# Kernel optimization log

Measured on AMD Instinct MI355X. Metric: run time of the kernel, lower is better.

Reference implementation:

```python
import jax, jax.numpy as jnp
import numpy as np
from jax import lax

B, C, H, W = 32, 256, 56, 56

def _conv(x, w, stride, groups=1, pad='VALID'):
    return lax.conv_general_dilated(x, w, (stride, stride), pad,
                                    feature_group_count=groups,
                                    dimension_numbers=('NCHW', 'OIHW', 'NCHW'))

def _ln(x, g, b, eps=1e-5):
    mu = jnp.mean(x, -1, keepdims=True)
    var = jnp.mean((x - mu) ** 2, -1, keepdims=True)
    return (x - mu) * lax.rsqrt(var + eps) * g + b

def setup_inputs() -> dict:
    key = jax.random.key(0)
    ks = jax.random.split(key, 16)
    s = 0.02
    Ch = C // 2
    d = {}
    d['x'] = jax.random.normal(ks[0], (B, C, H, W), jnp.float32)
    d['Wq'] = jax.random.normal(ks[1], (C, C), jnp.float32) * s;  d['bq'] = jnp.zeros((C,), jnp.float32)
    d['Wk'] = jax.random.normal(ks[2], (C, C), jnp.float32) * s;  d['bk'] = jnp.zeros((C,), jnp.float32)
    d['Wv'] = jax.random.normal(ks[3], (C, C), jnp.float32) * s;  d['bv'] = jnp.zeros((C,), jnp.float32)
    d['sr1_w'] = jax.random.normal(ks[4], (C, C, 8, 8), jnp.float32) * s; d['sr1_b'] = jnp.zeros((C,), jnp.float32)
    d['ln1_g'] = jnp.ones((C,), jnp.float32); d['ln1_b'] = jnp.zeros((C,), jnp.float32)
    d['sr2_w'] = jax.random.normal(ks[5], (C, C, 4, 4), jnp.float32) * s; d['sr2_b'] = jnp.zeros((C,), jnp.float32)
    d['ln2_g'] = jnp.ones((C,), jnp.float32); d['ln2_b'] = jnp.zeros((C,), jnp.float32)
    d['Wkv1'] = jax.random.normal(ks[6], (C, C), jnp.float32) * s; d['bkv1'] = jnp.zeros((C,), jnp.float32)
    d['Wkv2'] = jax.random.normal(ks[7], (C, C), jnp.float32) * s; d['bkv2'] = jnp.zeros((C,), jnp.float32)
    d['lc1_w'] = jax.random.normal(ks[8], (Ch, 1, 3, 3), jnp.float32) * s; d['lc1_b'] = jnp.zeros((Ch,), jnp.float32)
    d['lc2_w'] = jax.random.normal(ks[9], (Ch, 1, 3, 3), jnp.float32) * s; d['lc2_b'] = jnp.zeros((Ch,), jnp.float32)
    d['rp_w'] = jax.random.normal(ks[10], (C, C), jnp.float32) * s;  d['rp_b'] = jnp.zeros((C,), jnp.float32)
    d['rp12_w'] = jax.random.normal(ks[11], (C, C), jnp.float32) * s; d['rp12_b'] = jnp.zeros((C,), jnp.float32)
    d['dw_w'] = jax.random.normal(ks[12], (C, 2), jnp.float32) * 0.5  # Conv3d (2,1,1) depthwise, no bias
    return d

def reference(x, Wq, bq, Wk, bk, Wv, bv, sr1_w, sr1_b, ln1_g, ln1_b,
              sr2_w, sr2_b, ln2_g, ln2_b, Wkv1, bkv1, Wkv2, bkv2,
              lc1_w, lc1_b, lc2_w, lc2_b, rp_w, rp_b, rp12_w, rp12_b, dw_w):
    Bx, Cc, h, w = x.shape
    N = h * w
    Ch = Cc // 2
    xt = x.reshape(Bx, Cc, N).transpose(0, 2, 1)                 # [B,N,C]
    q = jax.nn.softmax(xt @ Wq + bq, axis=-1)                    # softmax over channels
    q1, q2 = q[..., :Ch], q[..., Ch:]

    # spatial-reduction branches (conv -> LN -> GELU)
    x1 = _conv(x, sr1_w, 8) + sr1_b[:, None, None]               # [B,C,7,7]
    x1 = jax.nn.gelu(_ln(x1.reshape(Bx, Cc, -1).transpose(0, 2, 1), ln1_g, ln1_b), approximate=False)
    x2 = _conv(x, sr2_w, 4) + sr2_b[:, None, None]               # [B,C,14,14]
    x2 = jax.nn.gelu(_ln(x2.reshape(Bx, Cc, -1).transpose(0, 2, 1), ln2_g, ln2_b), approximate=False)

    def branch(xr, Wkv, bkv, lc_w, lc_b, qh, hh):
        kv = (xr @ Wkv + bkv).reshape(Bx, -1, 2, Ch)
        k = jax.nn.softmax(kv[:, :, 0], axis=1)                  # softmax over reduced tokens
        v = kv[:, :, 1]
        vsp = v.transpose(0, 2, 1).reshape(Bx, Ch, hh, hh)
        v = v + (_conv(vsp, lc_w, 1, groups=Ch, pad='SAME') + lc_b[:, None, None]).reshape(Bx, Ch, -1).transpose(0, 2, 1)
        ctx = jnp.einsum('bnk,bnv->bkv', k, v)                   # [B,Ch,Ch]
        return jnp.einsum('bnk,bkv->bnv', qh, ctx)               # [B,N,Ch]

    a1 = branch(x1, Wkv1, bkv1, lc1_w, lc1_b, q1, 7)
    a2 = branch(x2, Wkv2, bkv2, lc2_w, lc2_b, q2, 14)
    eff2 = jnp.concatenate([a1, a2], axis=-1)                    # [B,N,C]
    eff2 = jnp.einsum('bni,oi->bon', eff2, rp12_w).reshape(Bx, Cc, h, w) + rp12_b[None, :, None, None]

    # global efficient-attention branch
    keys = jax.nn.softmax(xt @ Wk + bk, axis=1)                  # softmax over tokens
    values = xt @ Wv + bv
    ctx = jnp.einsum('bnk,bnv->bkv', keys, values)               # [B,C,C]
    att = jnp.einsum('bnk,bkv->bnv', q, ctx)                     # [B,N,C]
    eff = jnp.einsum('bni,oi->bon', att, rp_w).reshape(Bx, Cc, h, w) + rp_b[None, :, None, None]

    # Conv3d (2,1,1) depthwise merge over the two branches
    out = eff * dw_w[:, 0][None, :, None, None] + eff2 * dw_w[:, 1][None, :, None, None]
    return out
```

## Files before the change

kernel.cpp:

```cpp
#include <hip/hip_runtime.h>
#include <hip/hip_bf16.h>
#include <math.h>

#define B_ 32
#define H_ 56
#define W_ 56
#define N_ 3136
#define NT_ 100352

typedef short short8 __attribute__((ext_vector_type(8)));
typedef float f32x4 __attribute__((ext_vector_type(4)));

__device__ __forceinline__ unsigned short f2b(float f){
  union { float f; unsigned u; } v; v.f = f;
  return (unsigned short)((v.u + 0x7FFFu + ((v.u>>16)&1u)) >> 16);
}

#define LDSW(row, bo) ((unsigned)((row)*128 + ((bo) ^ (((row)&7)<<4))))

__device__ __forceinline__ short8 ldfrag(const char* base, int row, int kk){
  return *(const short8*)(base + LDSW(row, kk*2));
}
__device__ __forceinline__ f32x4 mfma16(short8 a, short8 b, f32x4 c){
  return __builtin_amdgcn_mfma_f32_16x16x32_bf16(a, b, c, 0, 0, 0);
}
__device__ __forceinline__ void gld16(void* lds, const void* g){
  __builtin_amdgcn_global_load_lds((__attribute__((address_space(1))) void*)g,
                                   (__attribute__((address_space(3))) void*)lds,
                                   16, 0, 0);
}

__global__ void prep_kernel(const float* __restrict__ Wq, const float* __restrict__ Wk,
                            const float* __restrict__ Wv, const float* __restrict__ Wkv1,
                            const float* __restrict__ Wkv2, const float* __restrict__ sr1w,
                            const float* __restrict__ sr2w, const float* __restrict__ rpw,
                            const float* __restrict__ rpb, const float* __restrict__ rp12w,
                            const float* __restrict__ rp12b, const float* __restrict__ dww,
                            unsigned short* WqT, unsigned short* WkT, unsigned short* WvT,
                            unsigned short* Wkv1T, unsigned short* Wkv2T,
                            unsigned short* srw1, unsigned short* srw2,
                            unsigned short* Acomb, float* bias_out)
{
  int idx = blockIdx.x*256 + threadIdx.x;
  const int total = 5*65536 + 4194304 + 1048576 + 131072 + 256;
  for (int i = idx; i < total; i += gridDim.x*256) {
    int j = i;
    if (j < 5*65536) {
      int w = j >> 16, e = j & 65535;
      int o = e >> 8, c = e & 255;
      const float* src = (w==0)?Wq:(w==1)?Wk:(w==2)?Wv:(w==3)?Wkv1:Wkv2;
      unsigned short* dst = (w==0)?WqT:(w==1)?WkT:(w==2)?WvT:(w==3)?Wkv1T:Wkv2T;
      dst[o*256+c] = f2b(src[c*256+o]);
      continue;
    }
    j -= 5*65536;
    if (j < 4194304) {
      int o = j >> 14, rem = j & 16383, pos = rem >> 8, c = rem & 255;
      srw1[j] = f2b(sr1w[o*16384 + c*64 + pos]);
      continue;
    }
    j -= 4194304;
    if (j < 1048576) {
      int o = j >> 12, rem = j & 4095, pos = rem >> 8, c = rem & 255;
      srw2[j] = f2b(sr2w[o*4096 + c*16 + pos]);
      continue;
    }
    j -= 1048576;
    if (j < 131072) {
      int o = j >> 9, i2 = j & 511;
      float v = (i2 < 256) ? dww[o*2+0]*rpw[o*256+i2]
                           : dww[o*2+1]*rp12w[o*256+(i2-256)];
      Acomb[o*512+i2] = f2b(v);
      continue;
    }
    j -= 131072;
    bias_out[j] = dww[j*2+0]*rpb[j] + dww[j*2+1]*rp12b[j];
  }
}

__global__ void transpose_kernel(const float* __restrict__ x, unsigned short* __restrict__ xt)
{
  __shared__ float tile[64][65];
  int bn = blockIdx.x; int b = bn / 49; int n0 = (bn - b*49)*64;
  int c0 = blockIdx.y*64;
  int t = threadIdx.x;
  {
    int cl = t >> 2, nq = t & 3;
    const float* src = x + ((size_t)(b*256 + c0 + cl))*N_ + n0 + nq*16;
#pragma unroll
    for (int j = 0; j < 4; j++){
      float4 v = *(const float4*)(src + j*4);
      tile[cl][nq*16 + j*4 + 0] = v.x;
      tile[cl][nq*16 + j*4 + 1] = v.y;
      tile[cl][nq*16 + j*4 + 2] = v.z;
      tile[cl][nq*16 + j*4 + 3] = v.w;
    }
  }
  __syncthreads();
  {
    int nl = t >> 2, cq = t & 3;
    unsigned short pk[16];
#pragma unroll
    for (int j=0;j<16;j++) pk[j] = f2b(tile[cq*16+j][nl]);
    unsigned short* dst = xt + ((size_t)(b*N_ + n0 + nl))*256 + c0 + cq*16;
    *(uint4*)dst = *(uint4*)&pk[0];
    *(uint4*)(dst+8) = *(uint4*)&pk[8];
  }
}

__global__ __launch_bounds__(256,2) void qkv3_kernel(
    const unsigned short* __restrict__ xt,
    const unsigned short* __restrict__ WqT, const unsigned short* __restrict__ WkT,
    const unsigned short* __restrict__ WvT,
    const float* __restrict__ bq, const float* __restrict__ bk, const float* __restrict__ bv,
    unsigned short* __restrict__ qbuf, unsigned short* __restrict__ KexpT,
    unsigned short* __restrict__ VT, float* __restrict__ s_q, float* __restrict__ s_k)
{
  __shared__ __align__(16) char smem[32768 + 32768 + 1024];
  char* At = smem;
  char* Bt = smem + 32768;
  float* redbuf = (float*)(smem + 65536);
  const int t = threadIdx.x, wave = t>>6, lane = t&63, l15 = lane&15, l4 = lane>>4;
  const int r0 = blockIdx.x*64;
  const int b = r0 / N_;
  const int nl0 = r0 - b*N_;

#pragma unroll
  for (int c4=0;c4<4;c4++)
#pragma unroll
    for (int j=0;j<2;j++){
      int chunk = j*256 + t; int row = chunk>>3, c8 = chunk&7;
      int c8s = c8 ^ (row&7);
      gld16(At + c4*8192 + (j*256 + wave*64)*16,
            xt + (size_t)(r0+row)*256 + c4*64 + c8s*8);
    }
  __syncthreads();

  for (int mat=0; mat<3; mat++){
    const unsigned short* BT = (mat==0)?WqT:(mat==1)?WkT:WvT;
    const float* bias = (mat==0)?bq:(mat==1)?bk:bv;
    const f32x4 vzero = {0.f,0.f,0.f,0.f};
    f32x4 acc[4][4];
#pragma unroll
    for (int i=0;i<4;i++)
#pragma unroll
      for (int j=0;j<4;j++) acc[i][j] = vzero;

    for (int k0c=0;k0c<4;k0c++){
#pragma unroll
      for (int j=0;j<8;j++){
        int chunk = j*256 + t; int row = chunk>>3, c8 = chunk&7;
        int c8s = c8 ^ (row&7);
        gld16(Bt + (j*256 + wave*64)*16, BT + (size_t)row*256 + k0c*64 + c8s*8);
      }
      __syncthreads();
#pragma unroll
      for (int ks=0;ks<2;ks++){
        short8 af[4], bfr[4];
#pragma unroll
        for (int mi=0;mi<4;mi++) af[mi]  = ldfrag(At + k0c*8192, mi*16 + l15, ks*32 + l4*8);
#pragma unroll
        for (int ni=0;ni<4;ni++) bfr[ni] = ldfrag(Bt, wave*64 + ni*16 + l15, ks*32 + l4*8);
#pragma unroll
        for (int mi=0;mi<4;mi++)
#pragma unroll
          for (int ni=0;ni<4;ni++)
            acc[mi][ni] = mfma16(af[mi], bfr[ni], acc[mi][ni]);
      }
      __syncthreads();
    }

    float bb4[4];
#pragma unroll
    for (int ni=0;ni<4;ni++) bb4[ni] = bias[wave*64 + ni*16 + l15];

    if (mat == 0) {
      float rs[4][4];
#pragma unroll
      for (int mi=0;mi<4;mi++)
#pragma unroll
        for (int r=0;r<4;r++) rs[mi][r] = 0.f;
#pragma unroll
      for (int mi=0;mi<4;mi++)
#pragma unroll
        for (int ni=0;ni<4;ni++)
#pragma unroll
          for (int r=0;r<4;r++){
            float e = __expf(acc[mi][ni][r] + bb4[ni]);
            acc[mi][ni][r] = e;
            rs[mi][r] += e;
          }
#pragma unroll
      for (int mi=0;mi<4;mi++)
#pragma unroll
        for (int r=0;r<4;r++){
          float s = rs[mi][r];
          s += __shfl_xor(s, 1); s += __shfl_xor(s, 2);
          s += __shfl_xor(s, 4); s += __shfl_xor(s, 8);
          rs[mi][r] = s;
        }
      if (l15 == 0){
#pragma unroll
        for (int mi=0;mi<4;mi++)
#pragma unroll
          for (int r=0;r<4;r++)
            redbuf[wave*64 + mi*16 + l4*4 + r] = rs[mi][r];
      }
      __syncthreads();
      unsigned short* qb = (unsigned short*)Bt;
#pragma unroll
      for (int mi=0;mi<4;mi++)
#pragma unroll
        for (int r=0;r<4;r++){
          int rr = mi*16 + l4*4 + r;
#pragma unroll
          for (int ni=0;ni<4;ni++)
            qb[rr*256 + wave*64 + ni*16 + l15] = f2b(acc[mi][ni][r]);
        }
      if (t < 64){
        s_q[r0 + t] = redbuf[t] + redbuf[64+t] + redbuf[128+t] + redbuf[192+t];
      }
      __syncthreads();
#pragma unroll
      for (int j=0;j<8;j++){
        int chunk = j*256 + t;
        int row = chunk >> 5, c8 = chunk & 31;
        *(uint4*)(qbuf + (size_t)(r0+row)*256 + c8*8) = *(const uint4*)(qb + row*256 + c8*8);
      }
      __syncthreads();
    } else {
      float cs[4] = {0.f,0.f,0.f,0.f};
#pragma unroll
      for (int mi=0;mi<4;mi++)
#pragma unroll
        for (int ni=0;ni<4;ni++)
#pragma unroll
          for (int r=0;r<4;r++){
            float v = acc[mi][ni][r] + bb4[ni];
            if (mat == 1){ v = __expf(v); cs[ni] += v; }
            int row = mi*16 + l4*4 + r;
            int col = wave*64 + ni*16 + l15;
            *(unsigned short*)(Bt + LDSW(col, row*2)) = f2b(v);
          }
      if (mat == 1){
#pragma unroll
        for (int ni=0;ni<4;ni++){
          float s = cs[ni];
          s += __shfl_xor(s, 16);
          s += __shfl_xor(s, 32);
          if (lane < 16) atomicAdd(&s_k[b*256 + wave*64 + ni*16 + lane], s);
        }
      }
      __syncthreads();
      unsigned short* ot = (mat==1) ? KexpT : VT;
#pragma unroll
      for (int j=0;j<8;j++){
        int chunk = j*256 + t;
        int c = chunk >> 3, n8 = chunk & 7;
        *(uint4*)(ot + ((size_t)b*256 + c)*N_ + nl0 + n8*8) = *(const uint4*)(Bt + LDSW(c, n8*16));
      }
      __syncthreads();
    }
  }
}

template<int S, int OW, int KW, int NSK, int MPB, int KTOT>
__device__ __forceinline__ void srconv_body(
    const unsigned short* __restrict__ xt, const unsigned short* __restrict__ wbf,
    float* __restrict__ part, int bid, char* At, char* Bt)
{
  const int KCH = KTOT / NSK;
  const int Mtot = B_*MPB;
  const int sk = bid % NSK, tile = bid / NSK;
  const int t = threadIdx.x, wave = t>>6, lane = t&63, l15 = lane&15, l4 = lane>>4;
  const f32x4 vzero = {0.f,0.f,0.f,0.f};
  f32x4 acc[4][4];
#pragma unroll
  for (int i=0;i<4;i++)
#pragma unroll
    for (int j=0;j<4;j++) acc[i][j] = vzero;

  size_t abase[2];
#pragma unroll
  for (int j=0;j<2;j++){
    int chunk = j*256 + t;
    int row = chunk >> 3, c8 = chunk & 7;
    int c8s = c8 ^ (row&7);
    int rowc = tile*64 + row; if (rowc > Mtot-1) rowc = Mtot-1;
    int b = rowc / MPB; int m = rowc - b*MPB;
    int p = m / OW; int q = m - p*OW;
    abase[j] = ((size_t)b*N_ + (size_t)(S*p)*W_ + S*q)*256 + c8s*8;
  }

  for (int kt = 0; kt < KCH; kt += 64){
    const int k0 = sk*KCH + kt;
    const int pos = k0 >> 8, cc = k0 & 255;
    const int dy = pos / KW, dx = pos - dy*KW;
    const size_t off = (size_t)(dy*W_ + dx)*256 + cc;
#pragma unroll
    for (int j=0;j<2;j++){
      gld16(At + (j*256 + wave*64)*16, xt + abase[j] + off);
    }
#pragma unroll
    for (int j=0;j<8;j++){
      int chunk = j*256 + t; int row = chunk>>3, c8 = chunk&7;
      int c8s = c8 ^ (row&7);
      gld16(Bt + (j*256 + wave*64)*16, wbf + (size_t)row*KTOT + k0 + c8s*8);
    }
    __syncthreads();
#pragma unroll
    for (int ks=0;ks<2;ks++){
      short8 af[4], bfr[4];
#pragma unroll
      for (int mi=0;mi<4;mi++) af[mi]  = ldfrag(At, mi*16 + l15, ks*32 + l4*8);
#pragma unroll
      for (int ni=0;ni<4;ni++) bfr[ni] = ldfrag(Bt, wave*64 + ni*16 + l15, ks*32 + l4*8);
#pragma unroll
      for (int mi=0;mi<4;mi++)
#pragma unroll
        for (int ni=0;ni<4;ni++)
          acc[mi][ni] = mfma16(af[mi], bfr[ni], acc[mi][ni]);
    }
    __syncthreads();
  }
#pragma unroll
  for (int mi=0;mi<4;mi++)
#pragma unroll
    for (int r=0;r<4;r++){
      int row = tile*64 + mi*16 + l4*4 + r;
      if (row < Mtot){
        size_t basep = ((size_t)sk*Mtot + row)*256;
#pragma unroll
        for (int ni=0;ni<4;ni++)
          part[basep + wave*64 + ni*16 + l15] = acc[mi][ni][r];
      }
    }
}

__device__ __forceinline__ void ctxmain_body(
    const unsigned short* __restrict__ KexpT, const unsigned short* __restrict__ VT,
    float* __restrict__ part, int idx, char* At, char* Bt)
{
  const int b = idx / 28; int rem = idx - b*28;
  const int y = rem / 7, sk = rem - y*7;
  const int mt = y >> 1, nt = y & 1;
  const int it0 = sk*7, it1 = it0+7;
  const int t = threadIdx.x;
  const int wave = t>>6, lane = t&63, l15 = lane&15, l4 = lane>>4;
  const int wm = (wave>>1)*64, wn = (wave&1)*64;
  const unsigned short* A  = KexpT + ((size_t)b*256 + mt*128)*N_;
  const unsigned short* Bv = VT + ((size_t)b*256 + nt*128)*N_;
  const f32x4 vzero = {0.f,0.f,0.f,0.f};
  f32x4 acc[4][4];
#pragma unroll
  for (int i=0;i<4;i++)
#pragma unroll
    for (int j=0;j<4;j++) acc[i][j] = vzero;

  for (int it=it0; it<it1; it++){
    const int k0 = it*64;
#pragma unroll
    for (int j=0;j<4;j++){
      int chunk = j*256 + t; int row = chunk>>3, c8 = chunk&7;
      int c8s = c8 ^ (row&7);
      gld16(At + (j*256 + wave*64)*16, A + (size_t)row*N_ + k0 + c8s*8);
    }
#pragma unroll
    for (int j=0;j<4;j++){
      int chunk = j*256 + t; int row = chunk>>3, c8 = chunk&7;
      int c8s = c8 ^ (row&7);
      gld16(Bt + (j*256 + wave*64)*16, Bv + (size_t)row*N_ + k0 + c8s*8);
    }
    __syncthreads();
#pragma unroll
    for (int ks=0;ks<2;ks++){
      short8 af[4], bfr[4];
#pragma unroll
      for (int mi=0;mi<4;mi++) af[mi]  = ldfrag(At, wm + mi*16 + l15, ks*32 + l4*8);
#pragma unroll
      for (int ni=0;ni<4;ni++) bfr[ni] = ldfrag(Bt, wn + ni*16 + l15, ks*32 + l4*8);
#pragma unroll
      for (int mi=0;mi<4;mi++)
#pragma unroll
        for (int ni=0;ni<4;ni++)
          acc[mi][ni] = mfma16(af[mi], bfr[ni], acc[mi][ni]);
    }
    __syncthreads();
  }
#pragma unroll
  for (int mi=0;mi<4;mi++)
#pragma unroll
    for (int r=0;r<4;r++){
      int kg = mt*128 + wm + mi*16 + l4*4 + r;
      size_t basep = (((size_t)sk*B_ + b)*256 + kg)*256 + nt*128 + wn;
#pragma unroll
      for (int ni=0;ni<4;ni++)
        part[basep + ni*16 + l15] = acc[mi][ni][r];
    }
}

__global__ __launch_bounds__(256,4) void conv_ctx_kernel(
    const unsigned short* __restrict__ xt, const unsigned short* __restrict__ srw1,
    const unsigned short* __restrict__ srw2, float* __restrict__ x1part,
    float* __restrict__ x2part, const unsigned short* __restrict__ KexpT,
    const unsigned short* __restrict__ VT, float* __restrict__ ctxpart)
{
  __shared__ __align__(16) char smem[8192 + 32768];
  if (blockIdx.x < 392)
    srconv_body<4,14,4,4,196,4096>(xt, srw2, x2part, blockIdx.x, smem, smem+8192);
  else if (blockIdx.x < 792)
    srconv_body<8,7,8,16,49,16384>(xt, srw1, x1part, blockIdx.x-392, smem, smem+8192);
  else
    ctxmain_body(KexpT, VT, ctxpart, blockIdx.x-792, smem, smem+16384);
}
// ... 232 lines not shown
  const int kk = kc*4 + kl;
  const float* kp = kexp + (size_t)b*M*128 + kk;
  const float* vp = vmod + (size_t)b*M*128 + j;
  float acc = 0.f, s = 0.f;
  for (int m = 0; m < M; m++){
    float kv = kp[(size_t)m*128];
    s += kv;
    acc += kv * vp[(size_t)m*128];
  }
  const int krow = BR ? (128+kk) : kk;
  unsigned short* dst = ctxcomb + ((size_t)b*256 + krow)*512;
  const int wbase = BR ? 384 : 256;
  const int zbase = BR ? 256 : 384;
  dst[wbase + j] = f2b(acc / s);
  dst[zbase + j] = 0;
}

__global__ __launch_bounds__(256,2) void final_kernel(
    const unsigned short* __restrict__ Gmat, const unsigned short* __restrict__ qbuf,
    const float* __restrict__ bias_out, const float* __restrict__ s_q,
    float* __restrict__ out)
{
  __shared__ __align__(16) char smem[16384 + 8192];
  char* At = smem; char* Bt = smem + 16384;
  const int b = blockIdx.x, ot = blockIdx.y, nt = blockIdx.z;
  const int t = threadIdx.x, wave = t>>6, lane = t&63, l15 = lane&15, l4 = lane>>4;
  const int wm = (wave>>1)*64, wn = (wave&1)*32;
  const unsigned short* A  = Gmat + ((size_t)b*256 + ot*128)*256;
  const unsigned short* Bq = qbuf + ((size_t)b*N_ + nt*64)*256;
  const f32x4 vzero = {0.f,0.f,0.f,0.f};
  f32x4 acc[4][2];
#pragma unroll
  for (int i=0;i<4;i++){ acc[i][0] = vzero; acc[i][1] = vzero; }

  for (int k0=0;k0<256;k0+=64){
#pragma unroll
    for (int j=0;j<4;j++){
      int chunk = j*256 + t; int row = chunk>>3, c8 = chunk&7;
      int c8s = c8 ^ (row&7);
      gld16(At + (j*256 + wave*64)*16, A + (size_t)row*256 + k0 + c8s*8);
    }
#pragma unroll
    for (int j=0;j<2;j++){
      int chunk = j*256 + t; int row = chunk>>3, c8 = chunk&7;
      int c8s = c8 ^ (row&7);
      gld16(Bt + (j*256 + wave*64)*16, Bq + (size_t)row*256 + k0 + c8s*8);
    }
    __syncthreads();
#pragma unroll
    for (int ks=0;ks<2;ks++){
      short8 af[4], bfr[2];
#pragma unroll
      for (int mi=0;mi<4;mi++) af[mi]  = ldfrag(At, wm + mi*16 + l15, ks*32 + l4*8);
#pragma unroll
      for (int ni=0;ni<2;ni++) bfr[ni] = ldfrag(Bt, wn + ni*16 + l15, ks*32 + l4*8);
#pragma unroll
      for (int mi=0;mi<4;mi++)
#pragma unroll
        for (int ni=0;ni<2;ni++)
          acc[mi][ni] = mfma16(af[mi], bfr[ni], acc[mi][ni]);
    }
    __syncthreads();
  }
  float iq[2];
#pragma unroll
  for (int ni=0;ni<2;ni++)
    iq[ni] = 1.0f / s_q[(size_t)b*N_ + nt*64 + wn + ni*16 + l15];
#pragma unroll
  for (int mi=0;mi<4;mi++)
#pragma unroll
    for (int r=0;r<4;r++){
      int o = ot*128 + wm + mi*16 + l4*4 + r;
      float bo = bias_out[o];
#pragma unroll
      for (int ni=0;ni<2;ni++){
        int n = nt*64 + wn + ni*16 + l15;
        out[((size_t)b*256 + o)*N_ + n] = acc[mi][ni][r]*iq[ni] + bo;
      }
    }
}

extern "C" void kernel_launch(void* const* d_in, const int* in_sizes, int n_in,
                              void* d_out, int out_size, void* d_ws, size_t ws_size,
                              hipStream_t stream)
{
  const float* x     = (const float*)d_in[0];
  const float* Wq    = (const float*)d_in[1];
  const float* bq    = (const float*)d_in[2];
  const float* Wk    = (const float*)d_in[3];
  const float* bk    = (const float*)d_in[4];
  const float* Wv    = (const float*)d_in[5];
  const float* bv    = (const float*)d_in[6];
  const float* sr1w  = (const float*)d_in[7];
  const float* sr1b  = (const float*)d_in[8];
  const float* ln1g  = (const float*)d_in[9];
  const float* ln1b  = (const float*)d_in[10];
  const float* sr2w  = (const float*)d_in[11];
  const float* sr2b  = (const float*)d_in[12];
  const float* ln2g  = (const float*)d_in[13];
  const float* ln2b  = (const float*)d_in[14];
  const float* Wkv1  = (const float*)d_in[15];
  const float* bkv1  = (const float*)d_in[16];
  const float* Wkv2  = (const float*)d_in[17];
  const float* bkv2  = (const float*)d_in[18];
  const float* lc1w  = (const float*)d_in[19];
  const float* lc1b  = (const float*)d_in[20];
  const float* lc2w  = (const float*)d_in[21];
  const float* lc2b  = (const float*)d_in[22];
  const float* rpw   = (const float*)d_in[23];
  const float* rpb   = (const float*)d_in[24];
  const float* rp12w = (const float*)d_in[25];
  const float* rp12b = (const float*)d_in[26];
  const float* dww   = (const float*)d_in[27];

  char* ws = (char*)d_ws;
  size_t off = 0;
  auto take = [&](size_t n)->char*{ char* p = ws + off; off += (n + 255) & ~(size_t)255; return p; };

  unsigned short* WqT   = (unsigned short*)take(131072);
  unsigned short* WkT   = (unsigned short*)take(131072);
  unsigned short* WvT   = (unsigned short*)take(131072);
  unsigned short* Wkv1T = (unsigned short*)take(131072);
  unsigned short* Wkv2T = (unsigned short*)take(131072);
  unsigned short* srw1  = (unsigned short*)take(8388608);
  unsigned short* srw2  = (unsigned short*)take(2097152);
  unsigned short* Acomb = (unsigned short*)take(262144);
  float* bias_out = (float*)take(1024);
  float* s_k      = (float*)take(32768);
  float* s_q      = (float*)take(401408);
  char* regionA = take(51380224);
  unsigned short* qbuf = (unsigned short*)take(51380224);
  char* regionK = take(51380224);
  char* regionV = take(51380224);
  float* x1part = (float*)take(25690112);
  if (off > ws_size) return;

  unsigned short* xt    = (unsigned short*)regionA;
  unsigned short* KexpT = (unsigned short*)regionK;
  unsigned short* VT = (unsigned short*)regionV;
  unsigned short* Gmat = (unsigned short*)regionV;
  unsigned short* x1g  = (unsigned short*)(regionV + 4194304);
  unsigned short* x2g  = (unsigned short*)(regionV + 4997120);
  float* kexp1 = (float*)(regionV + 8208384);
  float* vraw1 = (float*)(regionV + 9011200);
  float* vmod1 = (float*)(regionV + 9814016);
  float* kexp2 = (float*)(regionV + 10616832);
  float* vraw2 = (float*)(regionV + 13828096);
  float* vmod2 = (float*)(regionV + 17039360);
  unsigned short* ctxcomb = (unsigned short*)d_out;
  float* ctxpart = (float*)((char*)d_out + 8388608);
  float* x2part  = (float*)((char*)d_out + 67108864);

  hipMemsetAsync(s_k, 0, 32768, stream);
  prep_kernel<<<8192, 256, 0, stream>>>(Wq, Wk, Wv, Wkv1, Wkv2, sr1w, sr2w,
                                        rpw, rpb, rp12w, rp12b, dww,
                                        WqT, WkT, WvT, Wkv1T, Wkv2T, srw1, srw2,
                                        Acomb, bias_out);
  transpose_kernel<<<dim3(1568,4), 256, 0, stream>>>(x, xt);
  qkv3_kernel<<<1568, 256, 0, stream>>>(xt, WqT, WkT, WvT, bq, bk, bv,
                                        qbuf, KexpT, VT, s_q, s_k);
  conv_ctx_kernel<<<392+400+896, 256, 0, stream>>>(xt, srw1, srw2,
                                                   x1part, x2part, KexpT, VT, ctxpart);
  red_ln_kernel<<<7840+2048, 256, 0, stream>>>(x1part, x2part, sr1b, sr2b,
                                               ln1g, ln1b, ln2g, ln2b, x1g, x2g,
                                               ctxpart, s_k, ctxcomb);
  kv_both_kernel<<<123, 256, 0, stream>>>(x1g, Wkv1T, bkv1, kexp1, vraw1,
                                          x2g, Wkv2T, bkv2, kexp2, vraw2);
  dwconv_both_kernel<<<3920, 256, 0, stream>>>(vraw1, lc1w, lc1b, vmod1,
                                               vraw2, lc2w, lc2b, vmod2);
  ctxbr_both_kernel<<<dim3(32,64), 512, 0, stream>>>(kexp1, vmod1, kexp2, vmod2, ctxcomb);
  gmat_kernel<<<dim3(32,2,2), 256, 0, stream>>>(Acomb, ctxcomb, Gmat);
  final_kernel<<<dim3(32,2,49), 256, 0, stream>>>(Gmat, qbuf, bias_out, s_q, (float*)d_out);
}
```

Before: 424.0 us.

## Fuse transpose into prep kernel and split QKV GEMM into half-width chunks

```diff
diff --git a/kernel.cpp b/kernel.cpp
--- a/kernel.cpp
+++ b/kernel.cpp
@@ -30,20 +30,52 @@
                                    16, 0, 0);
 }
 
-__global__ void prep_kernel(const float* __restrict__ Wq, const float* __restrict__ Wk,
-                            const float* __restrict__ Wv, const float* __restrict__ Wkv1,
-                            const float* __restrict__ Wkv2, const float* __restrict__ sr1w,
-                            const float* __restrict__ sr2w, const float* __restrict__ rpw,
-                            const float* __restrict__ rpb, const float* __restrict__ rp12w,
-                            const float* __restrict__ rp12b, const float* __restrict__ dww,
-                            unsigned short* WqT, unsigned short* WkT, unsigned short* WvT,
-                            unsigned short* Wkv1T, unsigned short* Wkv2T,
-                            unsigned short* srw1, unsigned short* srw2,
-                            unsigned short* Acomb, float* bias_out)
-{
-  int idx = blockIdx.x*256 + threadIdx.x;
+__global__ void prep_trans_kernel(
+    const float* __restrict__ x, unsigned short* __restrict__ xt,
+    const float* __restrict__ Wq, const float* __restrict__ Wk,
+    const float* __restrict__ Wv, const float* __restrict__ Wkv1,
+    const float* __restrict__ Wkv2, const float* __restrict__ sr1w,
+    const float* __restrict__ sr2w, const float* __restrict__ rpw,
+    const float* __restrict__ rpb, const float* __restrict__ rp12w,
+    const float* __restrict__ rp12b, const float* __restrict__ dww,
+    unsigned short* WqT, unsigned short* WkT, unsigned short* WvT,
+    unsigned short* Wkv1T, unsigned short* Wkv2T,
+    unsigned short* srw1, unsigned short* srw2,
+    unsigned short* Acomb, float* bias_out)
+{
+  __shared__ float tile[64][65];
+  if (blockIdx.x < 6272){
+    int bn = blockIdx.x >> 2; int b = bn / 49; int n0 = (bn - b*49)*64;
+    int c0 = (blockIdx.x & 3)*64;
+    int t = threadIdx.x;
+    {
+      int cl = t >> 2, nq = t & 3;
+      const float* src = x + ((size_t)(b*256 + c0 + cl))*N_ + n0 + nq*16;
+#pragma unroll
+      for (int j = 0; j < 4; j++){
+        float4 v = *(const float4*)(src + j*4);
+        tile[cl][nq*16 + j*4 + 0] = v.x;
+        tile[cl][nq*16 + j*4 + 1] = v.y;
+        tile[cl][nq*16 + j*4 + 2] = v.z;
+        tile[cl][nq*16 + j*4 + 3] = v.w;
+      }
+    }
+    __syncthreads();
+    {
+      int nl = t >> 2, cq = t & 3;
+      unsigned short pk[16];
+#pragma unroll
+      for (int j=0;j<16;j++) pk[j] = f2b(tile[cq*16+j][nl]);
+      unsigned short* dst = xt + ((size_t)(b*N_ + n0 + nl))*256 + c0 + cq*16;
+      *(uint4*)dst = *(uint4*)&pk[0];
+      *(uint4*)(dst+8) = *(uint4*)&pk[8];
+    }
+    return;
+  }
+  int idx = (blockIdx.x - 6272)*256 + threadIdx.x;
+  const int stride = 2048*256;
   const int total = 5*65536 + 4194304 + 1048576 + 131072 + 256;
-  for (int i = idx; i < total; i += gridDim.x*256) {
+  for (int i = idx; i < total; i += stride) {
     int j = i;
     if (j < 5*65536) {
       int w = j >> 16, e = j & 65535;
@@ -78,37 +110,7 @@
   }
 }
 
-__global__ void transpose_kernel(const float* __restrict__ x, unsigned short* __restrict__ xt)
-{
-  __shared__ float tile[64][65];
-  int bn = blockIdx.x; int b = bn / 49; int n0 = (bn - b*49)*64;
-  int c0 = blockIdx.y*64;
-  int t = threadIdx.x;
-  {
-    int cl = t >> 2, nq = t & 3;
-    const float* src = x + ((size_t)(b*256 + c0 + cl))*N_ + n0 + nq*16;
-#pragma unroll
-    for (int j = 0; j < 4; j++){
-      float4 v = *(const float4*)(src + j*4);
-      tile[cl][nq*16 + j*4 + 0] = v.x;
-      tile[cl][nq*16 + j*4 + 1] = v.y;
-      tile[cl][nq*16 + j*4 + 2] = v.z;
-      tile[cl][nq*16 + j*4 + 3] = v.w;
-    }
-  }
-  __syncthreads();
-  {
-    int nl = t >> 2, cq = t & 3;
-    unsigned short pk[16];
-#pragma unroll
-    for (int j=0;j<16;j++) pk[j] = f2b(tile[cq*16+j][nl]);
-    unsigned short* dst = xt + ((size_t)(b*N_ + n0 + nl))*256 + c0 + cq*16;
-    *(uint4*)dst = *(uint4*)&pk[0];
-    *(uint4*)(dst+8) = *(uint4*)&pk[8];
-  }
-}
-
-__global__ __launch_bounds__(256,2) void qkv3_kernel(
+__global__ __launch_bounds__(256,3) void qkv6_kernel(
     const unsigned short* __restrict__ xt,
     const unsigned short* __restrict__ WqT, const unsigned short* __restrict__ WkT,
     const unsigned short* __restrict__ WvT,
@@ -116,10 +118,10 @@
     unsigned short* __restrict__ qbuf, unsigned short* __restrict__ KexpT,
     unsigned short* __restrict__ VT, float* __restrict__ s_q, float* __restrict__ s_k)
 {
-  __shared__ __align__(16) char smem[32768 + 32768 + 1024];
+  __shared__ __align__(16) char smem[32768 + 16384 + 1024];
   char* At = smem;
   char* Bt = smem + 32768;
-  float* redbuf = (float*)(smem + 65536);
+  float* redbuf = (float*)(smem + 49152);
   const int t = threadIdx.x, wave = t>>6, lane = t&63, l15 = lane&15, l4 = lane>>4;
   const int r0 = blockIdx.x*64;
   const int b = r0 / N_;
@@ -139,127 +141,128 @@
   for (int mat=0; mat<3; mat++){
     const unsigned short* BT = (mat==0)?WqT:(mat==1)?WkT:WvT;
     const float* bias = (mat==0)?bq:(mat==1)?bk:bv;
-    const f32x4 vzero = {0.f,0.f,0.f,0.f};
-    f32x4 acc[4][4];
-#pragma unroll
-    for (int i=0;i<4;i++)
-#pragma unroll
-      for (int j=0;j<4;j++) acc[i][j] = vzero;
-
-    for (int k0c=0;k0c<4;k0c++){
-#pragma unroll
-      for (int j=0;j<8;j++){
-        int chunk = j*256 + t; int row = chunk>>3, c8 = chunk&7;
-        int c8s = c8 ^ (row&7);
-        gld16(Bt + (j*256 + wave*64)*16, BT + (size_t)row*256 + k0c*64 + c8s*8);
+    float rs[4][4];
+#pragma unroll
+    for (int mi=0;mi<4;mi++)
+#pragma unroll
+      for (int r=0;r<4;r++) rs[mi][r] = 0.f;
+
+    for (int ch=0; ch<2; ch++){
+      const f32x4 vzero = {0.f,0.f,0.f,0.f};
+      f32x4 acc[4][2];
+#pragma unroll
+      for (int i=0;i<4;i++){ acc[i][0] = vzero; acc[i][1] = vzero; }
+
+      for (int k0c=0;k0c<4;k0c++){
+#pragma unroll
+        for (int j=0;j<4;j++){
+          int s = j*256 + t; int row = s>>3, c8 = s&7;
+          int c8s = c8 ^ (row&7);
+          gld16(Bt + (j*256 + wave*64)*16,
+                BT + (size_t)(ch*128 + row)*256 + k0c*64 + c8s*8);
+        }
+        __syncthreads();
+#pragma unroll
+        for (int ks=0;ks<2;ks++){
+          short8 af[4], bfr[2];
+#pragma unroll
+          for (int mi=0;mi<4;mi++)
+            af[mi] = ldfrag(At + k0c*8192, mi*16 + l15, ks*32 + l4*8);
+#pragma unroll
+          for (int ni=0;ni<2;ni++)
+            bfr[ni] = ldfrag(Bt, wave*32 + ni*16 + l15, ks*32 + l4*8);
+#pragma unroll
+          for (int mi=0;mi<4;mi++)
+#pragma unroll
+            for (int ni=0;ni<2;ni++)
+              acc[mi][ni] = mfma16(af[mi], bfr[ni], acc[mi][ni]);
+        }
+        __syncthreads();
       }
-      __syncthreads();
-#pragma unroll
-      for (int ks=0;ks<2;ks++){
-        short8 af[4], bfr[4];
-#pragma unroll
-        for (int mi=0;mi<4;mi++) af[mi]  = ldfrag(At + k0c*8192, mi*16 + l15, ks*32 + l4*8);
-#pragma unroll
-        for (int ni=0;ni<4;ni++) bfr[ni] = ldfrag(Bt, wave*64 + ni*16 + l15, ks*32 + l4*8);
+
+      float bb2[2];
+#pragma unroll
+      for (int ni=0;ni<2;ni++) bb2[ni] = bias[ch*128 + wave*32 + ni*16 + l15];
+
+      if (mat == 0){
 #pragma unroll
         for (int mi=0;mi<4;mi++)
 #pragma unroll
-          for (int ni=0;ni<4;ni++)
-            acc[mi][ni] = mfma16(af[mi], bfr[ni], acc[mi][ni]);
+          for (int ni=0;ni<2;ni++)
+#pragma unroll
+            for (int r=0;r<4;r++){
+              float e = __expf(acc[mi][ni][r] + bb2[ni]);
+              rs[mi][r] += e;
+              int row = mi*16 + l4*4 + r;
+              int cl = wave*32 + ni*16 + l15;
+              unsigned bo = (unsigned)((cl*2) ^ ((row&7)<<4));
+              *(unsigned short*)(Bt + row*256 + bo) = f2b(e);
+            }
+        __syncthreads();
+#pragma unroll
+        for (int j=0;j<4;j++){
+          int s = j*256 + t; int row = s>>4, c16 = s&15;
+          unsigned bo = (unsigned)((c16*16) ^ ((row&7)<<4));
+          *(uint4*)(qbuf + (size_t)(r0+row)*256 + ch*128 + c16*8) =
+              *(const uint4*)(Bt + row*256 + bo);
+        }
+        __syncthreads();
+        if (ch == 1){
+#pragma unroll
+          for (int mi=0;mi<4;mi++)
+#pragma unroll
+            for (int r=0;r<4;r++){
+              float s = rs[mi][r];
+              s += __shfl_xor(s, 1); s += __shfl_xor(s, 2);
+              s += __shfl_xor(s, 4); s += __shfl_xor(s, 8);
+              rs[mi][r] = s;
+            }
+          if (l15 == 0){
+#pragma unroll
+            for (int mi=0;mi<4;mi++)
+#pragma unroll
+              for (int r=0;r<4;r++)
+                redbuf[wave*64 + mi*16 + l4*4 + r] = rs[mi][r];
+          }
+          __syncthreads();
+          if (t < 64)
+            s_q[r0 + t] = redbuf[t] + redbuf[64+t] + redbuf[128+t] + redbuf[192+t];
+          __syncthreads();
+        }
+      } else {
+        float cs[2] = {0.f, 0.f};
+#pragma unroll
+        for (int mi=0;mi<4;mi++)
+#pragma unroll
+          for (int ni=0;ni<2;ni++)
+#pragma unroll
+            for (int r=0;r<4;r++){
+              float v = acc[mi][ni][r] + bb2[ni];
+              if (mat == 1){ v = __expf(v); cs[ni] += v; }
+              int row = mi*16 + l4*4 + r;
+              int cl = wave*32 + ni*16 + l15;
+              *(unsigned short*)(Bt + LDSW(cl, row*2)) = f2b(v);
+            }
+        if (mat == 1){
+#pragma unroll
+          for (int ni=0;ni<2;ni++){
+            float s = cs[ni];
+            s += __shfl_xor(s, 16);
+            s += __shfl_xor(s, 32);
+            if (lane < 16)
+              atomicAdd(&s_k[b*256 + ch*128 + wave*32 + ni*16 + lane], s);
+          }
+        }
+        __syncthreads();
+        unsigned short* ot = (mat==1) ? KexpT : VT;
+#pragma unroll
+        for (int j=0;j<4;j++){
+          int s = j*256 + t; int c = s>>3, n8 = s&7;
+          *(uint4*)(ot + ((size_t)b*256 + ch*128 + c)*N_ + nl0 + n8*8) =
+              *(const uint4*)(Bt + LDSW(c, n8*16));
+        }
+        __syncthreads();
       }
-      __syncthreads();
-    }
-
-    float bb4[4];
-#pragma unroll
-    for (int ni=0;ni<4;ni++) bb4[ni] = bias[wave*64 + ni*16 + l15];
-
-    if (mat == 0) {
-      float rs[4][4];
-#pragma unroll
-      for (int mi=0;mi<4;mi++)
-#pragma unroll
-        for (int r=0;r<4;r++) rs[mi][r] = 0.f;
-#pragma unroll
-      for (int mi=0;mi<4;mi++)
-#pragma unroll
-        for (int ni=0;ni<4;ni++)
-#pragma unroll
-          for (int r=0;r<4;r++){
-            float e = __expf(acc[mi][ni][r] + bb4[ni]);
-            acc[mi][ni][r] = e;
-            rs[mi][r] += e;
-          }
-#pragma unroll
-      for (int mi=0;mi<4;mi++)
-#pragma unroll
-        for (int r=0;r<4;r++){
-          float s = rs[mi][r];
-          s += __shfl_xor(s, 1); s += __shfl_xor(s, 2);
-          s += __shfl_xor(s, 4); s += __shfl_xor(s, 8);
-          rs[mi][r] = s;
-        }
-      if (l15 == 0){
-#pragma unroll
-        for (int mi=0;mi<4;mi++)
-#pragma unroll
-          for (int r=0;r<4;r++)
-            redbuf[wave*64 + mi*16 + l4*4 + r] = rs[mi][r];
-      }
-      __syncthreads();
-      unsigned short* qb = (unsigned short*)Bt;
-#pragma unroll
-      for (int mi=0;mi<4;mi++)
-#pragma unroll
-        for (int r=0;r<4;r++){
-          int rr = mi*16 + l4*4 + r;
-#pragma unroll
-          for (int ni=0;ni<4;ni++)
-            qb[rr*256 + wave*64 + ni*16 + l15] = f2b(acc[mi][ni][r]);
-        }
-      if (t < 64){
-        s_q[r0 + t] = redbuf[t] + redbuf[64+t] + redbuf[128+t] + redbuf[192+t];
-      }
-      __syncthreads();
-#pragma unroll
-      for (int j=0;j<8;j++){
-        int chunk = j*256 + t;
-        int row = chunk >> 5, c8 = chunk & 31;
-        *(uint4*)(qbuf + (size_t)(r0+row)*256 + c8*8) = *(const uint4*)(qb + row*256 + c8*8);
-      }
-      __syncthreads();
-    } else {
-      float cs[4] = {0.f,0.f,0.f,0.f};
-#pragma unroll
-      for (int mi=0;mi<4;mi++)
-#pragma unroll
-        for (int ni=0;ni<4;ni++)
-#pragma unroll
-          for (int r=0;r<4;r++){
-            float v = acc[mi][ni][r] + bb4[ni];
-            if (mat == 1){ v = __expf(v); cs[ni] += v; }
-            int row = mi*16 + l4*4 + r;
-            int col = wave*64 + ni*16 + l15;
-            *(unsigned short*)(Bt + LDSW(col, row*2)) = f2b(v);
-          }
-      if (mat == 1){
-#pragma unroll
-        for (int ni=0;ni<4;ni++){
-          float s = cs[ni];
-          s += __shfl_xor(s, 16);
-          s += __shfl_xor(s, 32);
-          if (lane < 16) atomicAdd(&s_k[b*256 + wave*64 + ni*16 + lane], s);
-        }
-      }
-      __syncthreads();
-      unsigned short* ot = (mat==1) ? KexpT : VT;
-#pragma unroll
-      for (int j=0;j<8;j++){
-        int chunk = j*256 + t;
-        int c = chunk >> 3, n8 = chunk & 7;
-        *(uint4*)(ot + ((size_t)b*256 + c)*N_ + nl0 + n8*8) = *(const uint4*)(Bt + LDSW(c, n8*16));
-      }
-      __syncthreads();
     }
   }
 }
@@ -798,12 +801,12 @@
   float* x2part  = (float*)((char*)d_out + 67108864);
 
   hipMemsetAsync(s_k, 0, 32768, stream);
-  prep_kernel<<<8192, 256, 0, stream>>>(Wq, Wk, Wv, Wkv1, Wkv2, sr1w, sr2w,
-                                        rpw, rpb, rp12w, rp12b, dww,
-                                        WqT, WkT, WvT, Wkv1T, Wkv2T, srw1, srw2,
-                                        Acomb, bias_out);
-  transpose_kernel<<<dim3(1568,4), 256, 0, stream>>>(x, xt);
-  qkv3_kernel<<<1568, 256, 0, stream>>>(xt, WqT, WkT, WvT, bq, bk, bv,
+  prep_trans_kernel<<<8320, 256, 0, stream>>>(x, xt,
+                                              Wq, Wk, Wv, Wkv1, Wkv2, sr1w, sr2w,
+                                              rpw, rpb, rp12w, rp12b, dww,
+                                              WqT, WkT, WvT, Wkv1T, Wkv2T, srw1, srw2,
+                                              Acomb, bias_out);
+  qkv6_kernel<<<1568, 256, 0, stream>>>(xt, WqT, WkT, WvT, bq, bk, bv,
                                         qbuf, KexpT, VT, s_q, s_k);
   conv_ctx_kernel<<<392+400+896, 256, 0, stream>>>(xt, srw1, srw2,
                                                    x1part, x2part, KexpT, VT, ctxpart);
```

Result: no change. 431.3 us (+1.7%).

## Fuse weight prep with input transpose and widen QKV kernel to 8 waves

Applied to the files above, without the earlier changes.

```diff
diff --git a/kernel.cpp b/kernel.cpp
--- a/kernel.cpp
+++ b/kernel.cpp
@@ -30,20 +30,52 @@
                                    16, 0, 0);
 }
 
-__global__ void prep_kernel(const float* __restrict__ Wq, const float* __restrict__ Wk,
-                            const float* __restrict__ Wv, const float* __restrict__ Wkv1,
-                            const float* __restrict__ Wkv2, const float* __restrict__ sr1w,
-                            const float* __restrict__ sr2w, const float* __restrict__ rpw,
-                            const float* __restrict__ rpb, const float* __restrict__ rp12w,
-                            const float* __restrict__ rp12b, const float* __restrict__ dww,
-                            unsigned short* WqT, unsigned short* WkT, unsigned short* WvT,
-                            unsigned short* Wkv1T, unsigned short* Wkv2T,
-                            unsigned short* srw1, unsigned short* srw2,
-                            unsigned short* Acomb, float* bias_out)
-{
-  int idx = blockIdx.x*256 + threadIdx.x;
+__global__ void prep_trans_kernel(
+    const float* __restrict__ x, unsigned short* __restrict__ xt,
+    const float* __restrict__ Wq, const float* __restrict__ Wk,
+    const float* __restrict__ Wv, const float* __restrict__ Wkv1,
+    const float* __restrict__ Wkv2, const float* __restrict__ sr1w,
+    const float* __restrict__ sr2w, const float* __restrict__ rpw,
+    const float* __restrict__ rpb, const float* __restrict__ rp12w,
+    const float* __restrict__ rp12b, const float* __restrict__ dww,
+    unsigned short* WqT, unsigned short* WkT, unsigned short* WvT,
+    unsigned short* Wkv1T, unsigned short* Wkv2T,
+    unsigned short* srw1, unsigned short* srw2,
+    unsigned short* Acomb, float* bias_out)
+{
+  __shared__ float tile[64][65];
+  if (blockIdx.x < 6272){
+    int bn = blockIdx.x >> 2; int b = bn / 49; int n0 = (bn - b*49)*64;
+    int c0 = (blockIdx.x & 3)*64;
+    int t = threadIdx.x;
+    {
+      int cl = t >> 2, nq = t & 3;
+      const float* src = x + ((size_t)(b*256 + c0 + cl))*N_ + n0 + nq*16;
+#pragma unroll
+      for (int j = 0; j < 4; j++){
+        float4 v = *(const float4*)(src + j*4);
+        tile[cl][nq*16 + j*4 + 0] = v.x;
+        tile[cl][nq*16 + j*4 + 1] = v.y;
+        tile[cl][nq*16 + j*4 + 2] = v.z;
+        tile[cl][nq*16 + j*4 + 3] = v.w;
+      }
+    }
+    __syncthreads();
+    {
+      int nl = t >> 2, cq = t & 3;
+      unsigned short pk[16];
+#pragma unroll
+      for (int j=0;j<16;j++) pk[j] = f2b(tile[cq*16+j][nl]);
+      unsigned short* dst = xt + ((size_t)(b*N_ + n0 + nl))*256 + c0 + cq*16;
+      *(uint4*)dst = *(uint4*)&pk[0];
+      *(uint4*)(dst+8) = *(uint4*)&pk[8];
+    }
+    return;
+  }
+  int idx = (blockIdx.x - 6272)*256 + threadIdx.x;
+  const int stride = 2048*256;
   const int total = 5*65536 + 4194304 + 1048576 + 131072 + 256;
-  for (int i = idx; i < total; i += gridDim.x*256) {
+  for (int i = idx; i < total; i += stride) {
     int j = i;
     if (j < 5*65536) {
       int w = j >> 16, e = j & 65535;
@@ -78,37 +110,7 @@
   }
 }
 
-__global__ void transpose_kernel(const float* __restrict__ x, unsigned short* __restrict__ xt)
-{
-  __shared__ float tile[64][65];
-  int bn = blockIdx.x; int b = bn / 49; int n0 = (bn - b*49)*64;
-  int c0 = blockIdx.y*64;
-  int t = threadIdx.x;
-  {
-    int cl = t >> 2, nq = t & 3;
-    const float* src = x + ((size_t)(b*256 + c0 + cl))*N_ + n0 + nq*16;
-#pragma unroll
-    for (int j = 0; j < 4; j++){
-      float4 v = *(const float4*)(src + j*4);
-      tile[cl][nq*16 + j*4 + 0] = v.x;
-      tile[cl][nq*16 + j*4 + 1] = v.y;
-      tile[cl][nq*16 + j*4 + 2] = v.z;
-      tile[cl][nq*16 + j*4 + 3] = v.w;
-    }
-  }
-  __syncthreads();
-  {
-    int nl = t >> 2, cq = t & 3;
-    unsigned short pk[16];
-#pragma unroll
-    for (int j=0;j<16;j++) pk[j] = f2b(tile[cq*16+j][nl]);
-    unsigned short* dst = xt + ((size_t)(b*N_ + n0 + nl))*256 + c0 + cq*16;
-    *(uint4*)dst = *(uint4*)&pk[0];
-    *(uint4*)(dst+8) = *(uint4*)&pk[8];
-  }
-}
-
-__global__ __launch_bounds__(256,2) void qkv3_kernel(
+__global__ __launch_bounds__(512,2) void qkv7_kernel(
     const unsigned short* __restrict__ xt,
     const unsigned short* __restrict__ WqT, const unsigned short* __restrict__ WkT,
     const unsigned short* __restrict__ WvT,
@@ -121,48 +123,47 @@
   char* Bt = smem + 32768;
   float* redbuf = (float*)(smem + 65536);
   const int t = threadIdx.x, wave = t>>6, lane = t&63, l15 = lane&15, l4 = lane>>4;
+  const int wm = (wave>>2)*32, wn = (wave&3)*64;
   const int r0 = blockIdx.x*64;
   const int b = r0 / N_;
   const int nl0 = r0 - b*N_;
 
 #pragma unroll
-  for (int c4=0;c4<4;c4++)
-#pragma unroll
-    for (int j=0;j<2;j++){
-      int chunk = j*256 + t; int row = chunk>>3, c8 = chunk&7;
-      int c8s = c8 ^ (row&7);
-      gld16(At + c4*8192 + (j*256 + wave*64)*16,
-            xt + (size_t)(r0+row)*256 + c4*64 + c8s*8);
-    }
+  for (int c4=0;c4<4;c4++){
+    int row = t>>3, c8 = t&7;
+    int c8s = c8 ^ (row&7);
+    gld16(At + c4*8192 + (size_t)t*16,
+          xt + (size_t)(r0+row)*256 + c4*64 + c8s*8);
+  }
   __syncthreads();
 
   for (int mat=0; mat<3; mat++){
     const unsigned short* BT = (mat==0)?WqT:(mat==1)?WkT:WvT;
     const float* bias = (mat==0)?bq:(mat==1)?bk:bv;
     const f32x4 vzero = {0.f,0.f,0.f,0.f};
-    f32x4 acc[4][4];
-#pragma unroll
-    for (int i=0;i<4;i++)
+    f32x4 acc[2][4];
+#pragma unroll
+    for (int i=0;i<2;i++)
 #pragma unroll
       for (int j=0;j<4;j++) acc[i][j] = vzero;
 
     for (int k0c=0;k0c<4;k0c++){
 #pragma unroll
-      for (int j=0;j<8;j++){
-        int chunk = j*256 + t; int row = chunk>>3, c8 = chunk&7;
+      for (int j=0;j<4;j++){
+        int chunk = j*512 + t; int row = chunk>>3, c8 = chunk&7;
         int c8s = c8 ^ (row&7);
-        gld16(Bt + (j*256 + wave*64)*16, BT + (size_t)row*256 + k0c*64 + c8s*8);
+        gld16(Bt + (size_t)chunk*16, BT + (size_t)row*256 + k0c*64 + c8s*8);
       }
       __syncthreads();
 #pragma unroll
       for (int ks=0;ks<2;ks++){
-        short8 af[4], bfr[4];
-#pragma unroll
-        for (int mi=0;mi<4;mi++) af[mi]  = ldfrag(At + k0c*8192, mi*16 + l15, ks*32 + l4*8);
-#pragma unroll
-        for (int ni=0;ni<4;ni++) bfr[ni] = ldfrag(Bt, wave*64 + ni*16 + l15, ks*32 + l4*8);
-#pragma unroll
-        for (int mi=0;mi<4;mi++)
+        short8 af[2], bfr[4];
+#pragma unroll
+        for (int mi=0;mi<2;mi++) af[mi]  = ldfrag(At + k0c*8192, wm + mi*16 + l15, ks*32 + l4*8);
+#pragma unroll
+        for (int ni=0;ni<4;ni++) bfr[ni] = ldfrag(Bt, wn + ni*16 + l15, ks*32 + l4*8);
+#pragma unroll
+        for (int mi=0;mi<2;mi++)
 #pragma unroll
           for (int ni=0;ni<4;ni++)
             acc[mi][ni] = mfma16(af[mi], bfr[ni], acc[mi][ni]);
@@ -172,16 +173,16 @@
 
     float bb4[4];
 #pragma unroll
-    for (int ni=0;ni<4;ni++) bb4[ni] = bias[wave*64 + ni*16 + l15];
+    for (int ni=0;ni<4;ni++) bb4[ni] = bias[wn + ni*16 + l15];
 
     if (mat == 0) {
-      float rs[4][4];
-#pragma unroll
-      for (int mi=0;mi<4;mi++)
+      float rs[2][4];
+#pragma unroll
+      for (int mi=0;mi<2;mi++)
 #pragma unroll
         for (int r=0;r<4;r++) rs[mi][r] = 0.f;
 #pragma unroll
-      for (int mi=0;mi<4;mi++)
+      for (int mi=0;mi<2;mi++)
 #pragma unroll
         for (int ni=0;ni<4;ni++)
 #pragma unroll
@@ -191,7 +192,7 @@
             rs[mi][r] += e;
           }
 #pragma unroll
-      for (int mi=0;mi<4;mi++)
+      for (int mi=0;mi<2;mi++)
 #pragma unroll
         for (int r=0;r<4;r++){
           float s = rs[mi][r];
@@ -201,45 +202,51 @@
         }
       if (l15 == 0){
 #pragma unroll
-        for (int mi=0;mi<4;mi++)
+        for (int mi=0;mi<2;mi++)
 #pragma unroll
           for (int r=0;r<4;r++)
-            redbuf[wave*64 + mi*16 + l4*4 + r] = rs[mi][r];
+            redbuf[wave*32 + mi*16 + l4*4 + r] = rs[mi][r];
       }
       __syncthreads();
       unsigned short* qb = (unsigned short*)Bt;
 #pragma unroll
-      for (int mi=0;mi<4;mi++)
+      for (int mi=0;mi<2;mi++)
 #pragma unroll
         for (int r=0;r<4;r++){
-          int rr = mi*16 + l4*4 + r;
-#pragma unroll
-          for (int ni=0;ni<4;ni++)
-            qb[rr*256 + wave*64 + ni*16 + l15] = f2b(acc[mi][ni][r]);
+          int rr = wm + mi*16 + l4*4 + r;
+#pragma unroll
+          for (int ni=0;ni<4;ni++){
+            int col = wn + ni*16 + l15;
+            unsigned bo = (unsigned)((col*2) ^ ((rr&7)<<4));
+            *(unsigned short*)((char*)qb + rr*512 + bo) = f2b(acc[mi][ni][r]);
+          }
         }
       if (t < 64){
-        s_q[r0 + t] = redbuf[t] + redbuf[64+t] + redbuf[128+t] + redbuf[192+t];
+        int g = t >> 5, local = t & 31;
+        s_q[r0 + t] = redbuf[(g*4+0)*32 + local] + redbuf[(g*4+1)*32 + local]
+                    + redbuf[(g*4+2)*32 + local] + redbuf[(g*4+3)*32 + local];
       }
       __syncthreads();
 #pragma unroll
-      for (int j=0;j<8;j++){
-        int chunk = j*256 + t;
-        int row = chunk >> 5, c8 = chunk & 31;
-        *(uint4*)(qbuf + (size_t)(r0+row)*256 + c8*8) = *(const uint4*)(qb + row*256 + c8*8);
+      for (int j=0;j<4;j++){
+        int chunk = j*512 + t;
+        int row = chunk >> 5, c16 = chunk & 31;
+        unsigned bo = (unsigned)((c16*16) ^ ((row&7)<<4));
+        *(uint4*)(qbuf + (size_t)(r0+row)*256 + c16*8) = *(const uint4*)((char*)qb + row*512 + bo);
       }
       __syncthreads();
     } else {
       float cs[4] = {0.f,0.f,0.f,0.f};
 #pragma unroll
-      for (int mi=0;mi<4;mi++)
+      for (int mi=0;mi<2;mi++)
 #pragma unroll
         for (int ni=0;ni<4;ni++)
 #pragma unroll
           for (int r=0;r<4;r++){
             float v = acc[mi][ni][r] + bb4[ni];
             if (mat == 1){ v = __expf(v); cs[ni] += v; }
-            int row = mi*16 + l4*4 + r;
-            int col = wave*64 + ni*16 + l15;
+            int row = wm + mi*16 + l4*4 + r;
+            int col = wn + ni*16 + l15;
             *(unsigned short*)(Bt + LDSW(col, row*2)) = f2b(v);
           }
       if (mat == 1){
@@ -248,14 +255,14 @@
           float s = cs[ni];
           s += __shfl_xor(s, 16);
           s += __shfl_xor(s, 32);
-          if (lane < 16) atomicAdd(&s_k[b*256 + wave*64 + ni*16 + lane], s);
+          if (lane < 16) atomicAdd(&s_k[b*256 + wn + ni*16 + lane], s);
         }
       }
       __syncthreads();
       unsigned short* ot = (mat==1) ? KexpT : VT;
 #pragma unroll
-      for (int j=0;j<8;j++){
-        int chunk = j*256 + t;
+      for (int j=0;j<4;j++){
+        int chunk = j*512 + t;
         int c = chunk >> 3, n8 = chunk & 7;
         *(uint4*)(ot + ((size_t)b*256 + c)*N_ + nl0 + n8*8) = *(const uint4*)(Bt + LDSW(c, n8*16));
       }
@@ -798,12 +805,12 @@
   float* x2part  = (float*)((char*)d_out + 67108864);
 
   hipMemsetAsync(s_k, 0, 32768, stream);
-  prep_kernel<<<8192, 256, 0, stream>>>(Wq, Wk, Wv, Wkv1, Wkv2, sr1w, sr2w,
-                                        rpw, rpb, rp12w, rp12b, dww,
-                                        WqT, WkT, WvT, Wkv1T, Wkv2T, srw1, srw2,
-                                        Acomb, bias_out);
-  transpose_kernel<<<dim3(1568,4), 256, 0, stream>>>(x, xt);
-  qkv3_kernel<<<1568, 256, 0, stream>>>(xt, WqT, WkT, WvT, bq, bk, bv,
+  prep_trans_kernel<<<8320, 256, 0, stream>>>(x, xt,
+                                              Wq, Wk, Wv, Wkv1, Wkv2, sr1w, sr2w,
+                                              rpw, rpb, rp12w, rp12b, dww,
+                                              WqT, WkT, WvT, Wkv1T, Wkv2T, srw1, srw2,
+                                              Acomb, bias_out);
+  qkv7_kernel<<<1568, 512, 0, stream>>>(xt, WqT, WkT, WvT, bq, bk, bv,
                                         qbuf, KexpT, VT, s_q, s_k);
   conv_ctx_kernel<<<392+400+896, 256, 0, stream>>>(xt, srw1, srw2,
                                                    x1part, x2part, KexpT, VT, ctxpart);
```

After: 441.1 us. +4.0%, slower.
